# Performance work log

Hardware: AMD Instinct MI355X
Metric: run time of the kernel (lower is better)

The kernel has to match this reference:

```python
import jax, jax.numpy as jnp
import numpy as np

CUTOFF = 5.0
MASK_VALUE = -1
N_POINTS = 1024
MAX_NEIGHBOURS = 128
_CELL = np.diag([20.0, 20.0, 20.0]).astype(np.float32)


def _cell_grid():
    # mirrors get_cell_list: integer image multiples bounding the cutoff sphere
    vol = abs(float(np.dot(_CELL[0], np.cross(_CELL[1], _CELL[2]))))
    maxes = []
    for v in range(3):
        clen = float(np.linalg.norm(np.cross(_CELL[(v + 1) % 3], _CELL[(v + 2) % 3])))
        maxes.append(int(np.ceil(CUTOFF / vol * clen)))
    g = np.array(np.meshgrid(np.arange(-maxes[0], maxes[0] + 1),
                             np.arange(-maxes[1], maxes[1] + 1),
                             np.arange(-maxes[2], maxes[2] + 1)))
    reshaped = g.T.reshape(-1, 3)  # (G, 3) integer cell shifts, G = 27 here
    return reshaped.astype(np.int32), reshaped.astype(np.float32) @ _CELL


def setup_inputs() -> dict:
    key = jax.random.key(0)
    cell_list, grid_points = _cell_grid()
    positions = jax.random.uniform(key, (N_POINTS, 3), dtype=jnp.float32, minval=0.0, maxval=20.0)
    return {
        'positions': positions,
        'grid_points': jnp.asarray(grid_points),
        'cell_list': jnp.asarray(cell_list),
        'max_neighbours': MAX_NEIGHBOURS,
    }


def reference(positions, grid_points, cell_list, max_neighbours):
    # Faithful translation of PeriodicBoundary.get_neighbours (include_self=False, include_images=True)
    n = positions.shape[0]
    # all periodic image copies of every point: (G*n, 3)
    neighbours = (grid_points[:, None, :] + positions[None, :, :]).reshape(-1, 3)
    # squared distances from every centre to every image point: (n, G*n)
    d2 = jnp.sum((neighbours[None, :, :] - positions[:, None, :]) ** 2, axis=-1)
    neigh_mask = d2 < CUTOFF * CUTOFF
    # exclude self-interaction (index j == i within the home cell block)
    self_mask = jnp.arange(neighbours.shape[0])[None, :] == jnp.arange(n, dtype=jnp.int32)[:, None]
    neigh_mask = neigh_mask & ~self_mask
    # per-row argwhere compaction into fixed-size padded neighbour lists
    to_idx = jax.vmap(lambda m: jnp.argwhere(m, size=max_neighbours, fill_value=MASK_VALUE))(neigh_mask)[..., 0]
    # cell shift for each flat image index: cells[j] = cell_list[j // n]
    cells = jnp.repeat(cell_list, n, axis=0)  # (G*n, 3)
    cell_indices = jax.vmap(jnp.take, (None, 0, None))(cells, to_idx, 0)  # (n, M, 3)
    neigh = jnp.where(to_idx == MASK_VALUE, MASK_VALUE, to_idx % n)  # (n, M)
    actual_max = jnp.max(neigh_mask.sum(axis=1))
    return neigh, cell_indices, actual_max
```

## Files before the change

### kernel.cpp

```cpp
#include <hip/hip_runtime.h>


#define NPTS 1024
#define MAXN 128
#define CUT2 25.0f
#define NTHR 512
#define NWAVE (NTHR / 64)
#define MAXCHUNK (NPTS / 64)

template <int NC>
__global__ __launch_bounds__(NTHR) void pb_fused(
    const float* __restrict__ positions,
    const float* __restrict__ grid_points,
    const int*   __restrict__ cell_list,
    int n, int G_rt,
    int* __restrict__ neigh,
    int* __restrict__ cells_out,
    int* __restrict__ actual_max)
{
    const int G = (NC > 0) ? NC : G_rt;
    const int nchunk = (n + 63) >> 6;

    __shared__ float4 sp[NPTS];
    __shared__ float4 sgrid[32];
    __shared__ int    scell[32][3];
    __shared__ unsigned long long smask[32][MAXCHUNK];
    __shared__ int    s_cnt[32];

    {
        float* spf = (float*)sp;
        const int n3 = n * 3;
        for (int j = threadIdx.x; j < n3; j += NTHR) {
            const int p = j / 3, c = j - 3 * p;
            spf[4 * p + c] = positions[j];
        }
        if (threadIdx.x < G) {
            sgrid[threadIdx.x] = make_float4(grid_points[3 * threadIdx.x + 0],
                                             grid_points[3 * threadIdx.x + 1],
                                             grid_points[3 * threadIdx.x + 2], 0.0f);
            scell[threadIdx.x][0] = cell_list[3 * threadIdx.x + 0];
            scell[threadIdx.x][1] = cell_list[3 * threadIdx.x + 1];
            scell[threadIdx.x][2] = cell_list[3 * threadIdx.x + 2];
        }
    }
    __syncthreads();

    const int i    = blockIdx.x;
    const int wid  = threadIdx.x >> 6;
    const int lane = threadIdx.x & 63;

    const float4 ci = sp[i];
    const float cx = ci.x, cy = ci.y, cz = ci.z;

    for (int c = wid; c < G; c += NWAVE) {
        const float4 g4 = sgrid[c];
        const float bx = fmaxf(fmaxf(g4.x - cx, cx - (g4.x + 20.0f)), 0.0f);
        const float by = fmaxf(fmaxf(g4.y - cy, cy - (g4.y + 20.0f)), 0.0f);
        const float bz = fmaxf(fmaxf(g4.z - cz, cz - (g4.z + 20.0f)), 0.0f);
        if (bx * bx + by * by + bz * bz < CUT2 + 1.0e-3f) {
            int cnt = 0;
#pragma unroll 4
            for (int ch = 0; ch < nchunk; ++ch) {
                const int p = (ch << 6) + lane;
                const float4 q = sp[p < n ? p : 0];
                float d2;
                {
#pragma clang fp contract(off)
                    const float ex = (g4.x + q.x) - cx;
                    const float ey = (g4.y + q.y) - cy;
                    const float ez = (g4.z + q.z) - cz;
                    d2 = (ex * ex + ey * ey) + ez * ez;
                }
                const bool pred = (p < n) && (d2 < CUT2) && (c * n + p != i);
                const unsigned long long m = __ballot(pred);
                if (lane == 0) smask[c][ch] = m;
                cnt += (int)__popcll(m);
            }
            if (lane == 0) s_cnt[c] = cnt;
        } else {
            if (lane < nchunk) smask[c][lane] = 0ull;
            if (lane == 0) s_cnt[c] = 0;
        }
    }
    __syncthreads();

    constexpr int JMAX = (NC > 0) ? (NC + NWAVE - 1) / NWAVE : 1;
    int offs[JMAX];
    int total = 0;
    if constexpr (NC > 0) {
        int run = 0;
#pragma unroll
        for (int c = 0; c < NC; ++c) {
            if ((c & (NWAVE - 1)) == wid) offs[c / NWAVE] = run;
            run += s_cnt[c];
        }
        total = run;
    } else {
        for (int c = 0; c < G; ++c) total += s_cnt[c];
    }

    int* __restrict__ nrow = neigh + (size_t)i * MAXN;
    int* __restrict__ crow = cells_out + (size_t)i * MAXN * 3;

    auto replay_cell = [&](int c, int offc) {
        const int c0 = scell[c][0], c1 = scell[c][1], c2 = scell[c][2];
        const unsigned long long lmask = (1ull << lane) - 1ull;
        int cursor = offc;
        for (int ch = 0; ch < nchunk; ++ch) {
            if (cursor >= MAXN) break;
            const unsigned long long m = smask[c][ch];
            if (!m) continue;
            const int before = __popcll(m & lmask);
            const int idx = cursor + before;
            if (((m >> lane) & 1ull) && idx < MAXN) {
                nrow[idx] = (ch << 6) + lane;
                crow[3 * idx + 0] = c0;
                crow[3 * idx + 1] = c1;
                crow[3 * idx + 2] = c2;
            }
            cursor += (int)__popcll(m);
        }
    };

    if constexpr (NC > 0) {
#pragma unroll
        for (int j = 0; j < JMAX; ++j) {
            const int c = wid + j * NWAVE;
            if (c >= NC) break;
            const int offc = offs[j];
            if (s_cnt[c] != 0 && offc < MAXN) replay_cell(c, offc);
        }
    } else {
        for (int c = wid; c < G; c += NWAVE) {
            int offc = 0;
            for (int cc = 0; cc < c; ++cc) offc += s_cnt[cc];
            if (s_cnt[c] != 0 && offc < MAXN) replay_cell(c, offc);
        }
    }

    const int f0 = scell[G - 1][0], f1 = scell[G - 1][1], f2 = scell[G - 1][2];
    const int base = total < MAXN ? total : MAXN;
    for (int kk = base + (int)threadIdx.x; kk < MAXN; kk += NTHR) {
        nrow[kk] = -1;
        crow[3 * kk + 0] = f0;
        crow[3 * kk + 1] = f1;
        crow[3 * kk + 2] = f2;
    }

    if (threadIdx.x == 0) atomicMax(actual_max, total);
}

extern "C" void kernel_launch(void* const* d_in, const int* in_sizes, int n_in,
                              void* d_out, int out_size, void* d_ws, size_t ws_size,
                              hipStream_t stream) {
    const float* positions   = (const float*)d_in[0];
    const float* grid_points = (const float*)d_in[1];
    const int*   cell_list   = (const int*)d_in[2];

    const int n = in_sizes[0] / 3;
    const int G = in_sizes[1] / 3;

    int* out        = (int*)d_out;
    int* neigh      = out;
    int* cells_out  = out + (size_t)n * MAXN;
    int* actual_max = out + (size_t)n * MAXN * 4;

    if (G == 27)
        pb_fused<27><<<n, NTHR, 0, stream>>>(positions, grid_points, cell_list,
                                             n, G, neigh, cells_out, actual_max);
    else
        pb_fused<0><<<n, NTHR, 0, stream>>>(positions, grid_points, cell_list,
                                            n, G, neigh, cells_out, actual_max);
}
```

Baseline: 23.05 us.

## Split chunk work across waves per surviving cell and parallelize offset scans

Cells that pass the bounding-box test are found with a single ballot, and every wave then processes a subset of chunks for each surviving cell instead of one wave owning a whole cell. Per-chunk and per-cell offsets are computed with shuffle-based prefix scans in shared memory, replacing serial per-wave counting. The aim is better load balance across waves when only a few cells are near the centre point. The cost is extra shared arrays, a mask-zeroing pass and additional barriers.

```diff
diff --git a/kernel.cpp b/kernel.cpp
--- a/kernel.cpp
+++ b/kernel.cpp
@@ -25,129 +25,139 @@
     __shared__ float4 sgrid[32];
     __shared__ int    scell[32][3];
     __shared__ unsigned long long smask[32][MAXCHUNK];
+    __shared__ int    s_choff[32][MAXCHUNK];
     __shared__ int    s_cnt[32];
+    __shared__ int    s_coff[32];
+    __shared__ int    s_total;
+
+    const int tid = threadIdx.x;
 
     {
         float* spf = (float*)sp;
         const int n3 = n * 3;
-        for (int j = threadIdx.x; j < n3; j += NTHR) {
+        for (int j = tid; j < n3; j += NTHR) {
             const int p = j / 3, c = j - 3 * p;
             spf[4 * p + c] = positions[j];
         }
-        if (threadIdx.x < G) {
-            sgrid[threadIdx.x] = make_float4(grid_points[3 * threadIdx.x + 0],
-                                             grid_points[3 * threadIdx.x + 1],
-                                             grid_points[3 * threadIdx.x + 2], 0.0f);
-            scell[threadIdx.x][0] = cell_list[3 * threadIdx.x + 0];
-            scell[threadIdx.x][1] = cell_list[3 * threadIdx.x + 1];
-            scell[threadIdx.x][2] = cell_list[3 * threadIdx.x + 2];
+        if (tid < G) {
+            sgrid[tid] = make_float4(grid_points[3 * tid + 0],
+                                     grid_points[3 * tid + 1],
+                                     grid_points[3 * tid + 2], 0.0f);
+            scell[tid][0] = cell_list[3 * tid + 0];
+            scell[tid][1] = cell_list[3 * tid + 1];
+            scell[tid][2] = cell_list[3 * tid + 2];
+        }
+        unsigned long long* smf = (unsigned long long*)smask;
+        for (int t = tid; t < G * MAXCHUNK; t += NTHR) smf[t] = 0ull;
+    }
+    __syncthreads();
+
+    const int i    = blockIdx.x;
+    const int wid  = tid >> 6;
+    const int lane = tid & 63;
+
+    const float4 ci = sp[i];
+    const float cx = ci.x, cy = ci.y, cz = ci.z;
+
+    unsigned long long svmask;
+    {
+        const float4 g4 = sgrid[lane < G ? lane : 0];
+        bool sv = false;
+        if (lane < G) {
+            const float bx = fmaxf(fmaxf(g4.x - cx, cx - (g4.x + 20.0f)), 0.0f);
+            const float by = fmaxf(fmaxf(g4.y - cy, cy - (g4.y + 20.0f)), 0.0f);
+            const float bz = fmaxf(fmaxf(g4.z - cz, cz - (g4.z + 20.0f)), 0.0f);
+            sv = (bx * bx + by * by + bz * bz < CUT2 + 1.0e-3f);
+        }
+        svmask = __ballot(sv);
+    }
+
+    for (unsigned long long m = svmask; m; m &= m - 1ull) {
+        const int c = (int)__builtin_ctzll(m);
+        const float4 g4 = sgrid[c];
+        for (int ch = wid; ch < nchunk; ch += NWAVE) {
+            const int p = (ch << 6) + lane;
+            const float4 q = sp[p < n ? p : 0];
+            float d2;
+            {
+#pragma clang fp contract(off)
+                const float ex = (g4.x + q.x) - cx;
+                const float ey = (g4.y + q.y) - cy;
+                const float ez = (g4.z + q.z) - cz;
+                d2 = (ex * ex + ey * ey) + ez * ez;
+            }
+            const bool pred = (p < n) && (d2 < CUT2) && (c * n + p != i);
+            const unsigned long long mm = __ballot(pred);
+            if (lane == 0) smask[c][ch] = mm;
         }
     }
     __syncthreads();
 
-    const int i    = blockIdx.x;
-    const int wid  = threadIdx.x >> 6;
-    const int lane = threadIdx.x & 63;
-
-    const float4 ci = sp[i];
-    const float cx = ci.x, cy = ci.y, cz = ci.z;
-
-    for (int c = wid; c < G; c += NWAVE) {
-        const float4 g4 = sgrid[c];
-        const float bx = fmaxf(fmaxf(g4.x - cx, cx - (g4.x + 20.0f)), 0.0f);
-        const float by = fmaxf(fmaxf(g4.y - cy, cy - (g4.y + 20.0f)), 0.0f);
-        const float bz = fmaxf(fmaxf(g4.z - cz, cz - (g4.z + 20.0f)), 0.0f);
-        if (bx * bx + by * by + bz * bz < CUT2 + 1.0e-3f) {
-            int cnt = 0;
-#pragma unroll 4
-            for (int ch = 0; ch < nchunk; ++ch) {
-                const int p = (ch << 6) + lane;
-                const float4 q = sp[p < n ? p : 0];
-                float d2;
-                {
-#pragma clang fp contract(off)
-                    const float ex = (g4.x + q.x) - cx;
-                    const float ey = (g4.y + q.y) - cy;
-                    const float ez = (g4.z + q.z) - cz;
-                    d2 = (ex * ex + ey * ey) + ez * ez;
-                }
-                const bool pred = (p < n) && (d2 < CUT2) && (c * n + p != i);
-                const unsigned long long m = __ballot(pred);
-                if (lane == 0) smask[c][ch] = m;
-                cnt += (int)__popcll(m);
-            }
-            if (lane == 0) s_cnt[c] = cnt;
-        } else {
-            if (lane < nchunk) smask[c][lane] = 0ull;
-            if (lane == 0) s_cnt[c] = 0;
+    if (tid < G * MAXCHUNK) {
+        const int c = tid >> 4, ch = tid & 15;
+        const int cnt = (ch < nchunk) ? (int)__popcll(smask[c][ch]) : 0;
+        int inc = cnt;
+#pragma unroll
+        for (int d = 1; d < 16; d <<= 1) {
+            const int v = __shfl_up(inc, d, 16);
+            if ((lane & 15) >= d) inc += v;
         }
+        s_choff[c][ch] = inc - cnt;
+        if (ch == 15) s_cnt[c] = inc;
     }
     __syncthreads();
 
-    constexpr int JMAX = (NC > 0) ? (NC + NWAVE - 1) / NWAVE : 1;
-    int offs[JMAX];
-    int total = 0;
-    if constexpr (NC > 0) {
-        int run = 0;
+    if (wid == 0) {
+        const int x = (lane < G) ? s_cnt[lane] : 0;
+        int inc = x;
 #pragma unroll
-        for (int c = 0; c < NC; ++c) {
-            if ((c & (NWAVE - 1)) == wid) offs[c / NWAVE] = run;
-            run += s_cnt[c];
+        for (int d = 1; d < 32; d <<= 1) {
+            const int v = __shfl_up(inc, d, 64);
+            if (lane >= d) inc += v;
         }
-        total = run;
-    } else {
-        for (int c = 0; c < G; ++c) total += s_cnt[c];
+        if (lane < G) s_coff[lane] = inc - x;
+        if (lane == G - 1) s_total = inc;
     }
+    __syncthreads();
 
     int* __restrict__ nrow = neigh + (size_t)i * MAXN;
     int* __restrict__ crow = cells_out + (size_t)i * MAXN * 3;
 
-    auto replay_cell = [&](int c, int offc) {
-        const int c0 = scell[c][0], c1 = scell[c][1], c2 = scell[c][2];
+    {
         const unsigned long long lmask = (1ull << lane) - 1ull;
-        int cursor = offc;
-        for (int ch = 0; ch < nchunk; ++ch) {
-            if (cursor >= MAXN) break;
-            const unsigned long long m = smask[c][ch];
-            if (!m) continue;
-            const int before = __popcll(m & lmask);
-            const int idx = cursor + before;
-            if (((m >> lane) & 1ull) && idx < MAXN) {
-                nrow[idx] = (ch << 6) + lane;
-                crow[3 * idx + 0] = c0;
-                crow[3 * idx + 1] = c1;
-                crow[3 * idx + 2] = c2;
+        for (unsigned long long m = svmask; m; m &= m - 1ull) {
+            const int c = (int)__builtin_ctzll(m);
+            const int offc = s_coff[c];
+            if (offc >= MAXN) continue;
+            const int c0 = scell[c][0], c1 = scell[c][1], c2 = scell[c][2];
+            for (int ch = wid; ch < nchunk; ch += NWAVE) {
+                const unsigned long long mm = smask[c][ch];
+                if (!mm) continue;
+                const int base2 = offc + s_choff[c][ch];
+                if (base2 >= MAXN) continue;
+                const int before = __popcll(mm & lmask);
+                const int idx = base2 + before;
+                if (((mm >> lane) & 1ull) && idx < MAXN) {
+                    nrow[idx] = (ch << 6) + lane;
+                    crow[3 * idx + 0] = c0;
+                    crow[3 * idx + 1] = c1;
+                    crow[3 * idx + 2] = c2;
+                }
             }
-            cursor += (int)__popcll(m);
-        }
-    };
-
-    if constexpr (NC > 0) {
-#pragma unroll
-        for (int j = 0; j < JMAX; ++j) {
-            const int c = wid + j * NWAVE;
-            if (c >= NC) break;
-            const int offc = offs[j];
-            if (s_cnt[c] != 0 && offc < MAXN) replay_cell(c, offc);
-        }
-    } else {
-        for (int c = wid; c < G; c += NWAVE) {
-            int offc = 0;
-            for (int cc = 0; cc < c; ++cc) offc += s_cnt[cc];
-            if (s_cnt[c] != 0 && offc < MAXN) replay_cell(c, offc);
         }
     }
 
+    const int total = s_total;
     const int f0 = scell[G - 1][0], f1 = scell[G - 1][1], f2 = scell[G - 1][2];
     const int base = total < MAXN ? total : MAXN;
-    for (int kk = base + (int)threadIdx.x; kk < MAXN; kk += NTHR) {
+    for (int kk = base + tid; kk < MAXN; kk += NTHR) {
         nrow[kk] = -1;
         crow[3 * kk + 0] = f0;
         crow[3 * kk + 1] = f1;
         crow[3 * kk + 2] = f2;
     }
 
-    if (threadIdx.x == 0) atomicMax(actual_max, total);
+    if (tid == 0) atomicMax(actual_max, total);
 }
 
 extern "C" void kernel_launch(void* const* d_in, const int* in_sizes, int n_in,
@@ -165,7 +175,7 @@
     int* cells_out  = out + (size_t)n * MAXN;
     int* actual_max = out + (size_t)n * MAXN * 4;
 
-    if (G == 27)
+    if (G == 27 && G * MAXCHUNK <= NTHR)
         pb_fused<27><<<n, NTHR, 0, stream>>>(positions, grid_points, cell_list,
                                              n, G, neigh, cells_out, actual_max);
     else
```

Result: faster. 21.02 us (-8.8%).
